# Performance work log

Hardware: AMD Instinct MI355X
Metric: run time of the kernel (lower is better)

Reference implementation:

```python
import jax, jax.numpy as jnp
import numpy as np

B, WIN, NN, NF, NH, NOUT = 4, 10, 10000, 8, 64, 1
N = B * WIN * NN          # stacked graph nodes
E = 3200000               # edges
EPS = 1e-5                # BatchNorm eps


def _gcn(x, edge_index, ew, W, b):
    # PyG GCNConv: linear first, then sym-normalized aggregation with self loops.
    xl = x @ W  # [N, H]
    loop = jnp.arange(N)
    row = jnp.concatenate([edge_index[0], loop])
    col = jnp.concatenate([edge_index[1], loop])
    w = jnp.concatenate([ew, jnp.ones((N,), ew.dtype)])
    deg = jax.ops.segment_sum(w, col, num_segments=N)
    dinv = jnp.where(deg > 0, jax.lax.rsqrt(deg), 0.0)
    norm = dinv[row] * w * dinv[col]
    out = jax.ops.segment_sum(norm[:, None] * xl[row], col, num_segments=N)
    return out + b


def _bn(x, g, bta):
    # training-mode BatchNorm1d (batch statistics, biased variance)
    m = x.mean(0)
    v = x.var(0)
    return (x - m) * jax.lax.rsqrt(v + EPS) * g + bta


def _lstm(xs, wih, whh, bih, bhh):
    # xs: [T, Bn, D]; PyTorch gate order i, f, g, o
    H = whh.shape[1]
    Bn = xs.shape[1]
    h0 = jnp.zeros((Bn, H), xs.dtype)
    c0 = jnp.zeros((Bn, H), xs.dtype)
    def step(carry, xt):
        h, c = carry
        gates = xt @ wih.T + bih + h @ whh.T + bhh
        i, f, g, o = jnp.split(gates, 4, axis=-1)
        c = jax.nn.sigmoid(f) * c + jax.nn.sigmoid(i) * jnp.tanh(g)
        h = jax.nn.sigmoid(o) * jnp.tanh(c)
        return (h, c), h
    (hn, cn), ys = jax.lax.scan(step, (h0, c0), xs)
    return ys, hn


def setup_inputs() -> dict:
    key = jax.random.key(0)
    ks = jax.random.split(key, 16)
    def rn(k, shape, s=0.05):
        return jax.random.normal(k, shape, jnp.float32) * s
    return {
        "x": jax.random.normal(ks[0], (N, NF), jnp.float32),
        "edge_index": jax.random.randint(ks[1], (2, E), 0, N),
        "edge_weight": jax.random.uniform(ks[2], (E,), jnp.float32),
        "c1_w": rn(ks[3], (NF, NH)), "c1_b": jnp.zeros((NH,), jnp.float32),
        "c2_w": rn(ks[4], (NH, NH)), "c2_b": jnp.zeros((NH,), jnp.float32),
        "bn1_g": jnp.ones((NH,), jnp.float32), "bn1_b": jnp.zeros((NH,), jnp.float32),
        "bn2_g": jnp.ones((NH,), jnp.float32), "bn2_b": jnp.zeros((NH,), jnp.float32),
        "l1_wih": rn(ks[5], (4 * NH, 2 * NH)), "l1_whh": rn(ks[6], (4 * NH, NH)),
        "l1_bih": jnp.zeros((4 * NH,), jnp.float32), "l1_bhh": jnp.zeros((4 * NH,), jnp.float32),
        "l2_wih": rn(ks[7], (4 * NH, NH)), "l2_whh": rn(ks[8], (4 * NH, NH)),
        "l2_bih": jnp.zeros((4 * NH,), jnp.float32), "l2_bhh": jnp.zeros((4 * NH,), jnp.float32),
        "fc1_w": rn(ks[9], (NH, 2 * NH + WIN * NF)), "fc1_b": jnp.zeros((NH,), jnp.float32),
        "fc2_w": rn(ks[10], (NOUT, NH)), "fc2_b": jnp.zeros((NOUT,), jnp.float32),
    }


def reference(x, edge_index, edge_weight, c1_w, c1_b, c2_w, c2_b,
              bn1_g, bn1_b, bn2_g, bn2_b,
              l1_wih, l1_whh, l1_bih, l1_bhh,
              l2_wih, l2_whh, l2_bih, l2_bhh,
              fc1_w, fc1_b, fc2_w, fc2_b):
    # skip connection: raw features per (batch,node) over the window
    skip = x.reshape(B, WIN, NN, NF).transpose(0, 2, 1, 3).reshape(B * NN, WIN * NF)
    # two GCN layers (dropout is identity in deterministic/eval reference)
    h1 = _bn(jax.nn.relu(_gcn(x, edge_index, edge_weight, c1_w, c1_b)), bn1_g, bn1_b)
    h2 = _bn(jax.nn.relu(_gcn(h1, edge_index, edge_weight, c2_w, c2_b)), bn2_g, bn2_b)
    xc = jnp.concatenate([h1, h2], axis=1)  # [N, 2H]
    xr = xc.reshape(B, WIN, NN, 2 * NH).transpose(1, 0, 2, 3).reshape(WIN, B * NN, 2 * NH)
    ys1, hn1 = _lstm(xr, l1_wih, l1_whh, l1_bih, l1_bhh)
    ys2, hn2 = _lstm(ys1, l2_wih, l2_whh, l2_bih, l2_bhh)
    z = jnp.concatenate([hn1, hn2, skip], axis=1)
    z = jax.nn.relu(z @ fc1_w.T + fc1_b)
    z = jax.nn.relu(z @ fc2_w.T + fc2_b)
    return z.reshape(-1)
```

## Files before the change

### kernel.cpp

```cpp
#include <hip/hip_runtime.h>
#include <math.h>

constexpr int BB     = 4;
constexpr int WINN   = 10;
constexpr int NNODES = 10000;
constexpr int NFEAT  = 8;
constexpr int NHID   = 64;
constexpr int NTOT   = BB * WINN * NNODES;
constexpr int NEDGE  = 3200000;
constexpr int NBN    = BB * NNODES;
constexpr float EPSBN = 1e-5f;

#define DEVFN static __device__ __forceinline__

typedef float f4 __attribute__((ext_vector_type(4)));
typedef short s8v __attribute__((ext_vector_type(8)));
typedef unsigned short ushort_t;
typedef unsigned int uint_t;

DEVFN float sigmoidf_(float x) { return 1.0f / (1.0f + __expf(-x)); }
DEVFN float tanhf_(float x) { return 2.0f / (1.0f + __expf(-2.0f * x)) - 1.0f; }
DEVFN ushort_t f2bf(float f) {
    uint_t x = __float_as_uint(f);
    return (ushort_t)((x + 0x7FFFu + ((x >> 16) & 1u)) >> 16);
}
DEVFN float bf2f(ushort_t u) { return __uint_as_float(((uint_t)u) << 16); }

__global__ void k_diag(float* out, float wsz, int n) {
    int i = blockIdx.x * 256 + threadIdx.x;
    if (i < n) out[i] = wsz;
}

__global__ void k_init(float* deg, int* cnt, float* sums) {
    int i = blockIdx.x * 256 + threadIdx.x;
    if (i < NTOT) { deg[i] = 1.0f; cnt[i] = 0; }
    if (i < 2048) sums[i] = 0.f;
}

__global__ void k_deg(const int* __restrict__ ei, const float* __restrict__ ew,
                      float* deg, int* cnt) {
    int e = blockIdx.x * 256 + threadIdx.x;
    if (e < NEDGE) {
        int c = ei[NEDGE + e];
        atomicAdd(&deg[c], ew[e]);
        atomicAdd(&cnt[c], 1);
    }
}

__global__ void k_dinv(float* deg) {
    int i = blockIdx.x * 256 + threadIdx.x;
    if (i < NTOT) { float d = deg[i]; deg[i] = (d > 0.f) ? rsqrtf(d) : 0.f; }
}

__global__ void k_scan1(const int* __restrict__ cnt, int* __restrict__ ptr, int* __restrict__ tmp) {
    __shared__ int sdat[256];
    int tid = threadIdx.x;
    int base = blockIdx.x * 1024 + tid * 4;
    int v0 = (base + 0 < NTOT) ? cnt[base + 0] : 0;
    int v1 = (base + 1 < NTOT) ? cnt[base + 1] : 0;
    int v2 = (base + 2 < NTOT) ? cnt[base + 2] : 0;
    int v3 = (base + 3 < NTOT) ? cnt[base + 3] : 0;
    int sum = v0 + v1 + v2 + v3;
    sdat[tid] = sum;
    __syncthreads();
    for (int ofs = 1; ofs < 256; ofs <<= 1) {
        int x = (tid >= ofs) ? sdat[tid - ofs] : 0;
        __syncthreads();
        sdat[tid] += x;
        __syncthreads();
    }
    int run = sdat[tid] - sum;
    if (base + 0 < NTOT) ptr[base + 0] = run; run += v0;
    if (base + 1 < NTOT) ptr[base + 1] = run; run += v1;
    if (base + 2 < NTOT) ptr[base + 2] = run; run += v2;
    if (base + 3 < NTOT) ptr[base + 3] = run;
    if (tid == 255) tmp[blockIdx.x] = sdat[255];
}

__global__ void k_scan2(int* tmp, int nb) {
    __shared__ int st[512];
    int tid = threadIdx.x;
    int v = (tid < nb) ? tmp[tid] : 0;
    st[tid] = v;
    __syncthreads();
    for (int ofs = 1; ofs < 512; ofs <<= 1) {
        int x = (tid >= ofs) ? st[tid - ofs] : 0;
        __syncthreads();
        st[tid] += x;
        __syncthreads();
    }
    if (tid < nb) tmp[tid] = st[tid] - v;
}

__global__ void k_scan3(int* __restrict__ ptr, int* __restrict__ cur, const int* __restrict__ tmp) {
    int i = blockIdx.x * 256 + threadIdx.x;
    if (i < NTOT) {
        int p = ptr[i] + tmp[i >> 10];
        ptr[i] = p;
        cur[i] = p;
    }
    if (i == 0) ptr[NTOT] = NEDGE;
}

__global__ void k_fill(const int* __restrict__ ei, const float* __restrict__ ew,
                       const float* __restrict__ dinv, int* __restrict__ cur,
                       int2* __restrict__ epack) {
    int e = blockIdx.x * 256 + threadIdx.x;
    if (e >= NEDGE) return;
    int row = ei[e], col = ei[NEDGE + e];
    float nv = dinv[row] * ew[e] * dinv[col];
    int pos = atomicAdd(&cur[col], 1);
    epack[pos] = make_int2(row, __float_as_int(nv));
}

__global__ void k_gather8(const int* __restrict__ ptr, const int2* __restrict__ epack,
                          const float* __restrict__ x, const float* __restrict__ dinv,
                          float* __restrict__ aggX) {
    int tid = threadIdx.x;
    int lane = tid & 63;
    int waveg = blockIdx.x * 4 + (tid >> 6);
    int g = lane >> 3, ch = lane & 7;
    int node = waveg * 8 + g;
    int beg = ptr[node], end = ptr[node + 1];
    float dv = dinv[node];
    float acc = dv * dv * x[node * 8 + ch];
    int e = beg;
    for (; e + 1 < end; e += 2) {
        int2 p0 = epack[e], p1 = epack[e + 1];
        acc = fmaf(__int_as_float(p0.y), x[p0.x * 8 + ch], acc);
        acc = fmaf(__int_as_float(p1.y), x[p1.x * 8 + ch], acc);
    }
    if (e < end) {
        int2 p = epack[e];
        acc = fmaf(__int_as_float(p.y), x[p.x * 8 + ch], acc);
    }
    aggX[node * 8 + ch] = acc;
}

__global__ void k_gather64(const int* __restrict__ ptr, const int2* __restrict__ epack,
                           const ushort_t* __restrict__ src, const float* __restrict__ dinv,
                           float* __restrict__ dst) {
    int lane = threadIdx.x & 63;
    int node = blockIdx.x * 4 + (threadIdx.x >> 6);
    int beg = ptr[node], end = ptr[node + 1];
    float dv = dinv[node];
    float acc = dv * dv * bf2f(src[(size_t)node * 64 + lane]);
    int e = beg;
    for (; e + 1 < end; e += 2) {
        int2 p0 = epack[e], p1 = epack[e + 1];
        acc = fmaf(__int_as_float(p0.y), bf2f(src[(size_t)p0.x * 64 + lane]), acc);
        acc = fmaf(__int_as_float(p1.y), bf2f(src[(size_t)p1.x * 64 + lane]), acc);
    }
    if (e < end) {
        int2 p = epack[e];
        acc = fmaf(__int_as_float(p.y), bf2f(src[(size_t)p.x * 64 + lane]), acc);
    }
    dst[(size_t)node * 64 + lane] = acc;
}

__global__ void k_lin1(const float* __restrict__ aggX, const float* __restrict__ W,
                       const float* __restrict__ bias, float* __restrict__ h1,
                       float* __restrict__ sums) {
    __shared__ float sW[NFEAT * NHID];
    int tid = threadIdx.x;
    sW[tid] = W[tid];
    sW[tid + 256] = W[tid + 256];
    __syncthreads();
    int c = tid & 63;
    float b = bias[c];
    float s = 0.f, sq = 0.f;
    int stride = gridDim.x * 256;
    for (int i = blockIdx.x * 256 + tid; i < NTOT * 64; i += stride) {
        int n = i >> 6;
        float acc = b;
#pragma unroll
        for (int f = 0; f < NFEAT; ++f) acc = fmaf(aggX[n * NFEAT + f], sW[f * NHID + c], acc);
        acc = acc > 0.f ? acc : 0.f;
        h1[i] = acc;
        s += acc;
        sq = fmaf(acc, acc, sq);
    }
    __shared__ float ls[4][64], lq[4][64];
    int w = tid >> 6;
    ls[w][c] = s; lq[w][c] = sq;
    __syncthreads();
    if (tid < 64) {
        atomicAdd(&sums[tid], ls[0][tid] + ls[1][tid] + ls[2][tid] + ls[3][tid]);
        atomicAdd(&sums[64 + tid], lq[0][tid] + lq[1][tid] + lq[2][tid] + lq[3][tid]);
    }
}

__global__ void k_bn_final(const float* __restrict__ sums, const float* __restrict__ g,
                           const float* __restrict__ b, float* __restrict__ ss) {
    int i = threadIdx.x;
    if (i >= 64) return;
    float mean = sums[i] * (1.0f / NTOT);
    float var = sums[64 + i] * (1.0f / NTOT) - mean * mean;
    float sc = g[i] * rsqrtf(var + EPSBN);
    ss[i] = sc;
    ss[64 + i] = b[i] - mean * sc;
}

__global__ void k_bn_final8(const float* __restrict__ sums8, const float* __restrict__ g,
                            const float* __restrict__ b, float* __restrict__ ss) {
    int i = threadIdx.x;
    if (i >= 64) return;
    float S = 0.f, Q = 0.f;
#pragma unroll
    for (int m = 0; m < 8; ++m) { S += sums8[m * 128 + i]; Q += sums8[m * 128 + 64 + i]; }
    float mean = S * (1.0f / NTOT);
    float var = Q * (1.0f / NTOT) - mean * mean;
    float sc = g[i] * rsqrtf(var + EPSBN);
    ss[i] = sc;
    ss[64 + i] = b[i] - mean * sc;
}

__global__ void k_bn1cast(const float* __restrict__ pre, const float* __restrict__ ss,
                          ushort_t* __restrict__ dst) {
    int c = threadIdx.x & 63;
    float sc = ss[c], sh = ss[64 + c];
    int stride = gridDim.x * 256;
    for (int i = blockIdx.x * 256 + threadIdx.x; i < NTOT * 64; i += stride)
        dst[i] = f2bf(fmaf(pre[i], sc, sh));
}

__global__ void k_lin2b(const float* __restrict__ io, const float* __restrict__ W2,
                        const float* __restrict__ bias, ushort_t* __restrict__ dst,
                        float* __restrict__ sums8) {
    __shared__ __align__(16) float srow[4][64];
    __shared__ float ls[4][64], lq[4][64];
    int lane = threadIdx.x & 63, wv = threadIdx.x >> 6;
    float wc[64];
#pragma unroll
    for (int h = 0; h < 64; ++h) wc[h] = W2[h * 64 + lane];
    float b = bias[lane];
    float s = 0.f, sq = 0.f;
    int wid = blockIdx.x * 4 + wv;
    int nw = gridDim.x * 4;
    for (int row = wid; row < NTOT; row += nw) {
        const float* hr = io + (size_t)row * 64;
        srow[wv][lane] = hr[lane];
        float acc = b;
#pragma unroll
        for (int h4 = 0; h4 < 16; ++h4) {
            float4 iv = *reinterpret_cast<const float4*>(&srow[wv][h4 * 4]);
            acc = fmaf(iv.x, wc[h4 * 4 + 0], acc);
            acc = fmaf(iv.y, wc[h4 * 4 + 1], acc);
            acc = fmaf(iv.z, wc[h4 * 4 + 2], acc);
            acc = fmaf(iv.w, wc[h4 * 4 + 3], acc);
        }
        acc = acc > 0.f ? acc : 0.f;
        dst[(size_t)row * 64 + lane] = f2bf(acc);
        s += acc;
        sq = fmaf(acc, acc, sq);
    }
    ls[wv][lane] = s; lq[wv][lane] = sq;
    __syncthreads();
    if (threadIdx.x < 64) {
        float S = ls[0][lane] + ls[1][lane] + ls[2][lane] + ls[3][lane];
        float Q = lq[0][lane] + lq[1][lane] + lq[2][lane] + lq[3][lane];
        float* d = sums8 + (blockIdx.x & 7) * 128;
        atomicAdd(&d[lane], S);
        atomicAdd(&d[64 + lane], Q);
    }
}

__global__ void k_prep(const float* __restrict__ wih1, const float* __restrict__ whh1,
                       const float* __restrict__ bih1, const float* __restrict__ bhh1,
                       const float* __restrict__ wih2, const float* __restrict__ whh2,
                       const float* __restrict__ bih2, const float* __restrict__ bhh2,
                       const float* __restrict__ fc1w,
                       float* wB1f, float* b1, ushort_t* wB2h, float* b2, float* fc1T) {
    int i = blockIdx.x * 256 + threadIdx.x;
    if (i < 256 * 192) {
        int n = i / 192, k = i - n * 192;
        wB1f[i] = (k < 128) ? wih1[n * 128 + k] : whh1[n * 64 + (k - 128)];
    }
    if (i < 256 * 128) {
        int n = i >> 7, k = i & 127;
        wB2h[i] = f2bf((k < 64) ? wih2[n * 64 + k] : whh2[n * 64 + (k - 64)]);
    }
    if (i < 208 * 64) {
        int k = i >> 6, o = i & 63;
        fc1T[i] = fc1w[o * 208 + k];
    }
    if (i < 256) { b1[i] = bih1[i] + bhh1[i]; b2[i] = bih2[i] + bhh2[i]; }
}

__global__ void k_fold2(float* __restrict__ wB1f, float* __restrict__ b1,
                        const float* __restrict__ ss2, ushort_t* __restrict__ wB1h) {
    int n = threadIdx.x;
    float acc = 0.f;
#pragma unroll
    for (int m = 0; m < 64; ++m) {
        float w = wB1f[n * 192 + 64 + m];
        acc = fmaf(w, ss2[64 + m], acc);
        wB1f[n * 192 + 64 + m] = w * ss2[m];
    }
    b1[n] += acc;
    __syncthreads();
    for (int j = n; j < 256 * 192; j += 256) wB1h[j] = f2bf(wB1f[j]);
}

__global__ __launch_bounds__(256, 2) void k_lstm_mfma4(
    const ushort_t* __restrict__ h1bf, const ushort_t* __restrict__ h2bf,
    const ushort_t* __restrict__ wB1, const ushort_t* __restrict__ wB2,
    const float* __restrict__ bs1, const float* __restrict__ bs2,
    float* __restrict__ hA, float* __restrict__ hB) {
    __shared__ ushort_t hx1[1024], hx2[1024];
    int tid = threadIdx.x;
    int lane = tid & 63, wv = tid >> 6;
    int c15 = lane & 15, g4 = lane >> 4;
    int g8 = g4 * 8;
    int bn0 = blockIdx.x * 16;
    int b = bn0 / NNODES, nn0 = bn0 - b * NNODES;

    for (int i = tid; i < 512; i += 256) { ((uint_t*)hx1)[i] = 0u; ((uint_t*)hx2)[i] = 0u; }

    s8v w1f[4][6], w2f[4][4];
#pragma unroll
    for (int j = 0; j < 4; ++j) {
        const ushort_t* base1 = wB1 + (size_t)((wv + 4 * j) * 16 + c15) * 192 + g8;
#pragma unroll
        for (int kk = 0; kk < 6; ++kk) w1f[j][kk] = *(const s8v*)(base1 + kk * 32);
        const ushort_t* base2 = wB2 + (size_t)((wv + 4 * j) * 16 + c15) * 128 + g8;
#pragma unroll
        for (int kk = 0; kk < 4; ++kk) w2f[j][kk] = *(const s8v*)(base2 + kk * 32);
    }
    float bi1[4], bi2[4];
#pragma unroll
    for (int j = 0; j < 4; ++j) {
        bi1[j] = bs1[(wv + 4 * j) * 16 + c15];
        bi2[j] = bs2[(wv + 4 * j) * 16 + c15];
    }
    float cA[4], cB[4];
#pragma unroll
    for (int q = 0; q < 4; ++q) { cA[q] = 0.f; cB[q] = 0.f; }

    int r7 = c15 & 7;
    int a_lo = c15 * 64 + ((g4 ^ r7) << 3);
    int a_hi = c15 * 64 + (((4 + g4) ^ r7) << 3);
    int u = wv * 16 + c15;
    int hxcol_hi = (u >> 3) << 3;
    int u7 = u & 7;

    __syncthreads();

    for (int t = 0; t < WINN; ++t) {
        size_t node = (size_t)((b * WINN + t) * NNODES + nn0 + c15) * 64 + g8;
        s8v a[6];
        a[0] = *(const s8v*)(h1bf + node);
        a[1] = *(const s8v*)(h1bf + node + 32);
        a[2] = *(const s8v*)(h2bf + node);
        a[3] = *(const s8v*)(h2bf + node + 32);
        a[4] = *(const s8v*)(&hx1[a_lo]);
        a[5] = *(const s8v*)(&hx1[a_hi]);

        f4 acc[4];
#pragma unroll
        for (int j = 0; j < 4; ++j) { f4 v = {bi1[j], bi1[j], bi1[j], bi1[j]}; acc[j] = v; }
#pragma unroll
        for (int j = 0; j < 4; ++j)
#pragma unroll
            for (int kk = 0; kk < 6; ++kk)
                acc[j] = __builtin_amdgcn_mfma_f32_16x16x32_bf16(a[kk], w1f[j][kk], acc[j], 0, 0, 0);
        __syncthreads();
#pragma unroll
        for (int q = 0; q < 4; ++q) {
            float ig = sigmoidf_(acc[0][q]);
            float fg = sigmoidf_(acc[1][q]);
            float gg = tanhf_(acc[2][q]);
            float og = sigmoidf_(acc[3][q]);
            float cv = fmaf(fg, cA[q], ig * gg);
            cA[q] = cv;
            float hv = og * tanhf_(cv);
            int rr = g4 * 4 + q;
            hx1[rr * 64 + (hxcol_hi ^ ((rr & 7) << 3)) + u7] = f2bf(hv);
        }
        __syncthreads();

        s8v r[4];
        r[0] = *(const s8v*)(&hx1[a_lo]);
        r[1] = *(const s8v*)(&hx1[a_hi]);
        r[2] = *(const s8v*)(&hx2[a_lo]);
        r[3] = *(const s8v*)(&hx2[a_hi]);
#pragma unroll
        for (int j = 0; j < 4; ++j) { f4 v = {bi2[j], bi2[j], bi2[j], bi2[j]}; acc[j] = v; }
#pragma unroll
        for (int j = 0; j < 4; ++j)
#pragma unroll
            for (int kk = 0; kk < 4; ++kk)
                acc[j] = __builtin_amdgcn_mfma_f32_16x16x32_bf16(r[kk], w2f[j][kk], acc[j], 0, 0, 0);
        __syncthreads();
#pragma unroll
        for (int q = 0; q < 4; ++q) {
            float ig = sigmoidf_(acc[0][q]);
            float fg = sigmoidf_(acc[1][q]);
            float gg = tanhf_(acc[2][q]);
            float og = sigmoidf_(acc[3][q]);
            float cv = fmaf(fg, cB[q], ig * gg);
            cB[q] = cv;
            float hv = og * tanhf_(cv);
            int rr = g4 * 4 + q;
            hx2[rr * 64 + (hxcol_hi ^ ((rr & 7) << 3)) + u7] = f2bf(hv);
        }
        __syncthreads();
    }
    for (int i = tid; i < 1024; i += 256) {
        int rr = i >> 6, uu = i & 63;
        int hw = rr * 64 + ((((uu >> 3) ^ (rr & 7)) << 3)) + (uu & 7);
        hA[(size_t)(bn0 + rr) * 64 + uu] = bf2f(hx1[hw]);
        hB[(size_t)(bn0 + rr) * 64 + uu] = bf2f(hx2[hw]);
    }
}

__global__ void k_head(const float* __restrict__ hA, const float* __restrict__ hB,
                       const float* __restrict__ x, const float* __restrict__ fc1T,
                       const float* __restrict__ fc1b, const float* __restrict__ fc2w,
                       const float* __restrict__ fc2b, float* __restrict__ out) {
    int lane = threadIdx.x & 63, wv = threadIdx.x >> 6;
    int bn = blockIdx.x * 4 + wv;
    __shared__ float sz[4][208];
    int b = bn / NNODES, nn = bn - b * NNODES;
    for (int k = lane; k < 208; k += 64) {
        float v;
        if (k < 64) v = hA[(size_t)bn * 64 + k];
        else if (k < 128) v = hB[(size_t)bn * 64 + (k - 64)];
        else {
            int kk = k - 128;
            int w = kk >> 3, f = kk & 7;
            v = x[(size_t)((b * WINN + w) * NNODES + nn) * NFEAT + f];
        }
        sz[wv][k] = v;
    }
    __syncthreads();
    float acc = fc1b[lane];
    for (int k = 0; k < 208; ++k) acc = fmaf(sz[wv][k], fc1T[k * 64 + lane], acc);
    acc = acc > 0.f ? acc : 0.f;
    float v = acc * fc2w[lane];
#pragma unroll
    for (int m = 32; m >= 1; m >>= 1) v += __shfl_xor(v, m, 64);
    if (lane == 0) {
        float z = v + fc2b[0];
        out[bn] = z > 0.f ? z : 0.f;
    }
}

extern "C" void kernel_launch(void* const* d_in, const int* in_sizes, int n_in,
                              void* d_out, int out_size, void* d_ws, size_t ws_size,
                              hipStream_t stream) {
    const float* x     = (const float*)d_in[0];
    const int*   ei    = (const int*)d_in[1];
    const float* ew    = (const float*)d_in[2];
    const float* c1w   = (const float*)d_in[3];
    const float* c1b   = (const float*)d_in[4];
    const float* c2w   = (const float*)d_in[5];
    const float* c2b   = (const float*)d_in[6];
    const float* bn1g  = (const float*)d_in[7];
    const float* bn1b  = (const float*)d_in[8];
    const float* bn2g  = (const float*)d_in[9];
    const float* bn2b  = (const float*)d_in[10];
    const float* wih1  = (const float*)d_in[11];
    const float* whh1  = (const float*)d_in[12];
    const float* bih1  = (const float*)d_in[13];
    const float* bhh1  = (const float*)d_in[14];
    const float* wih2  = (const float*)d_in[15];
    const float* whh2  = (const float*)d_in[16];
    const float* bih2  = (const float*)d_in[17];
    const float* bhh2  = (const float*)d_in[18];
    const float* fc1w  = (const float*)d_in[19];
    const float* fc1b  = (const float*)d_in[20];
    const float* fc2w  = (const float*)d_in[21];
    const float* fc2b  = (const float*)d_in[22];
    float* out = (float*)d_out;

    float* ws = (float*)d_ws;
    size_t off = 0;
    auto A = [&](size_t n) { float* p = ws + off; off += n; return p; };
    float* dinv   = A(NTOT);
    float* aggX   = A((size_t)NTOT * NFEAT);
    float* big    = A((size_t)NTOT * 64);
    ushort_t* h1bf = (ushort_t*)A((size_t)NTOT * 32);
    ushort_t* h2bf = (ushort_t*)A((size_t)NTOT * 32);

    size_t uoff = off;
    float* hA = A((size_t)NBN * 64);
    float* hB = A((size_t)NBN * 64);
    A(2 * (size_t)NEDGE + 2 * NTOT + 2 - 2 * (size_t)NBN * 64);
    int2* epack = (int2*)(ws + uoff);
    int*  ptr   = (int*)(epack + NEDGE);
    int*  cur   = ptr + NTOT + 1;

    float* wB1f = A(256 * 192);
    ushort_t* wB1h = (ushort_t*)A(256 * 96);
    ushort_t* wB2h = (ushort_t*)A(256 * 64);
    float* b1   = A(256);
    float* b2   = A(256);
    float* fc1T = A(208 * 64);
    float* sums = A(2048);
    float* ss1  = A(128);
    float* ss2  = A(128);
    float* scanTmpF = A(512);
    int* scanTmp = (int*)scanTmpF;

    if (ws_size < off * sizeof(float)) {
        k_diag<<<(out_size + 255) / 256, 256, 0, stream>>>(out, (float)ws_size, out_size);
        return;
    }

    constexpr int SCAN_NB = (NTOT + 1023) / 1024;

    k_init<<<(NTOT + 255) / 256, 256, 0, stream>>>(dinv, cur, sums);
    k_deg<<<NEDGE / 256, 256, 0, stream>>>(ei, ew, dinv, cur);
    k_dinv<<<(NTOT + 255) / 256, 256, 0, stream>>>(dinv);
    k_scan1<<<SCAN_NB, 256, 0, stream>>>(cur, ptr, scanTmp);
    k_scan2<<<1, 512, 0, stream>>>(scanTmp, SCAN_NB);
    k_scan3<<<(NTOT + 255) / 256, 256, 0, stream>>>(ptr, cur, scanTmp);
    k_fill<<<NEDGE / 256, 256, 0, stream>>>(ei, ew, dinv, cur, epack);
    k_prep<<<192, 256, 0, stream>>>(wih1, whh1, bih1, bhh1, wih2, whh2, bih2, bhh2,
                                    fc1w, wB1f, b1, wB2h, b2, fc1T);

    k_gather8<<<NTOT / 8 / 4, 256, 0, stream>>>(ptr, epack, x, dinv, aggX);
    k_lin1<<<512, 256, 0, stream>>>(aggX, c1w, c1b, big, sums);
    k_bn_final<<<1, 64, 0, stream>>>(sums, bn1g, bn1b, ss1);
    k_bn1cast<<<2048, 256, 0, stream>>>(big, ss1, h1bf);

    k_gather64<<<NTOT / 4, 256, 0, stream>>>(ptr, epack, h1bf, dinv, big);
    k_lin2b<<<2048, 256, 0, stream>>>(big, c2w, c2b, h2bf, sums + 128);
    k_bn_final8<<<1, 64, 0, stream>>>(sums + 128, bn2g, bn2b, ss2);
    k_fold2<<<1, 256, 0, stream>>>(wB1f, b1, ss2, wB1h);

    k_lstm_mfma4<<<NBN / 16, 256, 0, stream>>>(h1bf, h2bf, wB1h, wB2h, b1, b2, hA, hB);

    k_head<<<NBN / 4, 256, 0, stream>>>(hA, hB, x, fc1T, fc1b, fc2w, fc2b, out);
}
```

Before: 1.217 ms.

## Privatize CSR build counters into 8 partitions and compute degree from CSR

Replaces the float and int atomic degree and count pass with a single integer histogram split across 8 partitioned counter copies, chosen by block index, to spread atomic contention. Degree is then computed deterministically from the built CSR by a segmented reduction, and the per-edge normalization moves into the gather kernels, which now also load dinv[row] for every edge. This removes the float atomics and the dinv kernel. In exchange it adds 8x counter memory and initialization, an extra CSR pass, and an extra random dinv load per edge in both gathers.

```diff
diff --git a/kernel.cpp b/kernel.cpp
--- a/kernel.cpp
+++ b/kernel.cpp
@@ -31,36 +31,34 @@
     if (i < n) out[i] = wsz;
 }
 
-__global__ void k_init(float* deg, int* cnt, float* sums) {
+__global__ void k_init(int* cntP, float* sums) {
     int i = blockIdx.x * 256 + threadIdx.x;
-    if (i < NTOT) { deg[i] = 1.0f; cnt[i] = 0; }
+    if (i < 8 * NTOT) cntP[i] = 0;
     if (i < 2048) sums[i] = 0.f;
 }
 
-__global__ void k_deg(const int* __restrict__ ei, const float* __restrict__ ew,
-                      float* deg, int* cnt) {
+__global__ void k_hist(const int* __restrict__ ei, int* __restrict__ cntP) {
     int e = blockIdx.x * 256 + threadIdx.x;
-    if (e < NEDGE) {
-        int c = ei[NEDGE + e];
-        atomicAdd(&deg[c], ew[e]);
-        atomicAdd(&cnt[c], 1);
-    }
-}
-
-__global__ void k_dinv(float* deg) {
-    int i = blockIdx.x * 256 + threadIdx.x;
-    if (i < NTOT) { float d = deg[i]; deg[i] = (d > 0.f) ? rsqrtf(d) : 0.f; }
-}
-
-__global__ void k_scan1(const int* __restrict__ cnt, int* __restrict__ ptr, int* __restrict__ tmp) {
+    int p = blockIdx.x & 7;
+    if (e < NEDGE) atomicAdd(&cntP[p * NTOT + ei[NEDGE + e]], 1);
+}
+
+__global__ void k_scan1(const int* __restrict__ cntP, int* __restrict__ ptr, int* __restrict__ tmp) {
     __shared__ int sdat[256];
     int tid = threadIdx.x;
     int base = blockIdx.x * 1024 + tid * 4;
-    int v0 = (base + 0 < NTOT) ? cnt[base + 0] : 0;
-    int v1 = (base + 1 < NTOT) ? cnt[base + 1] : 0;
-    int v2 = (base + 2 < NTOT) ? cnt[base + 2] : 0;
-    int v3 = (base + 3 < NTOT) ? cnt[base + 3] : 0;
-    int sum = v0 + v1 + v2 + v3;
+    int v[4];
+#pragma unroll
+    for (int j = 0; j < 4; ++j) {
+        int idx = base + j;
+        int s = 0;
+        if (idx < NTOT) {
+#pragma unroll
+            for (int p = 0; p < 8; ++p) s += cntP[p * NTOT + idx];
+        }
+        v[j] = s;
+    }
+    int sum = v[0] + v[1] + v[2] + v[3];
     sdat[tid] = sum;
     __syncthreads();
     for (int ofs = 1; ofs < 256; ofs <<= 1) {
@@ -70,9 +68,9 @@
         __syncthreads();
     }
     int run = sdat[tid] - sum;
-    if (base + 0 < NTOT) ptr[base + 0] = run; run += v0;
-    if (base + 1 < NTOT) ptr[base + 1] = run; run += v1;
-    if (base + 2 < NTOT) ptr[base + 2] = run; run += v2;
+    if (base + 0 < NTOT) ptr[base + 0] = run; run += v[0];
+    if (base + 1 < NTOT) ptr[base + 1] = run; run += v[1];
+    if (base + 2 < NTOT) ptr[base + 2] = run; run += v[2];
     if (base + 3 < NTOT) ptr[base + 3] = run;
     if (tid == 255) tmp[blockIdx.x] = sdat[255];
 }
@@ -92,25 +90,46 @@
     if (tid < nb) tmp[tid] = st[tid] - v;
 }
 
-__global__ void k_scan3(int* __restrict__ ptr, int* __restrict__ cur, const int* __restrict__ tmp) {
+__global__ void k_scan3(int* __restrict__ ptr, int* __restrict__ cntP, const int* __restrict__ tmp) {
     int i = blockIdx.x * 256 + threadIdx.x;
     if (i < NTOT) {
-        int p = ptr[i] + tmp[i >> 10];
-        ptr[i] = p;
-        cur[i] = p;
+        int p0 = ptr[i] + tmp[i >> 10];
+        ptr[i] = p0;
+        int run = p0;
+#pragma unroll
+        for (int p = 0; p < 8; ++p) {
+            int c = cntP[p * NTOT + i];
+            cntP[p * NTOT + i] = run;
+            run += c;
+        }
     }
     if (i == 0) ptr[NTOT] = NEDGE;
 }
 
 __global__ void k_fill(const int* __restrict__ ei, const float* __restrict__ ew,
-                       const float* __restrict__ dinv, int* __restrict__ cur,
-                       int2* __restrict__ epack) {
+                       int* __restrict__ cur8, int2* __restrict__ epack) {
     int e = blockIdx.x * 256 + threadIdx.x;
     if (e >= NEDGE) return;
+    int p = blockIdx.x & 7;
     int row = ei[e], col = ei[NEDGE + e];
-    float nv = dinv[row] * ew[e] * dinv[col];
-    int pos = atomicAdd(&cur[col], 1);
-    epack[pos] = make_int2(row, __float_as_int(nv));
+    int pos = atomicAdd(&cur8[p * NTOT + col], 1);
+    epack[pos] = make_int2(row, __float_as_int(ew[e]));
+}
+
+__global__ void k_degcsr(const int* __restrict__ ptr, const int2* __restrict__ epack,
+                         float* __restrict__ dinv) {
+    int tid = threadIdx.x;
+    int lane = tid & 63;
+    int waveg = blockIdx.x * 4 + (tid >> 6);
+    int g = lane >> 3, sub = lane & 7;
+    int node = waveg * 8 + g;
+    int beg = ptr[node], end = ptr[node + 1];
+    float s = 0.f;
+    for (int e = beg + sub; e < end; e += 8) s += __int_as_float(epack[e].y);
+    s += __shfl_xor(s, 1, 64);
+    s += __shfl_xor(s, 2, 64);
+    s += __shfl_xor(s, 4, 64);
+    if (sub == 0) dinv[node] = rsqrtf(1.0f + s);
 }
 
 __global__ void k_gather8(const int* __restrict__ ptr, const int2* __restrict__ epack,
@@ -123,18 +142,18 @@
     int node = waveg * 8 + g;
     int beg = ptr[node], end = ptr[node + 1];
     float dv = dinv[node];
-    float acc = dv * dv * x[node * 8 + ch];
+    float accE = 0.f;
     int e = beg;
     for (; e + 1 < end; e += 2) {
         int2 p0 = epack[e], p1 = epack[e + 1];
-        acc = fmaf(__int_as_float(p0.y), x[p0.x * 8 + ch], acc);
-        acc = fmaf(__int_as_float(p1.y), x[p1.x * 8 + ch], acc);
+        accE = fmaf(dinv[p0.x] * __int_as_float(p0.y), x[p0.x * 8 + ch], accE);
+        accE = fmaf(dinv[p1.x] * __int_as_float(p1.y), x[p1.x * 8 + ch], accE);
     }
     if (e < end) {
         int2 p = epack[e];
-        acc = fmaf(__int_as_float(p.y), x[p.x * 8 + ch], acc);
-    }
-    aggX[node * 8 + ch] = acc;
+        accE = fmaf(dinv[p.x] * __int_as_float(p.y), x[p.x * 8 + ch], accE);
+    }
+    aggX[node * 8 + ch] = dv * fmaf(dv, x[node * 8 + ch], accE);
 }
 
 __global__ void k_gather64(const int* __restrict__ ptr, const int2* __restrict__ epack,
@@ -144,18 +163,18 @@
     int node = blockIdx.x * 4 + (threadIdx.x >> 6);
     int beg = ptr[node], end = ptr[node + 1];
     float dv = dinv[node];
-    float acc = dv * dv * bf2f(src[(size_t)node * 64 + lane]);
+    float accE = 0.f;
     int e = beg;
     for (; e + 1 < end; e += 2) {
         int2 p0 = epack[e], p1 = epack[e + 1];
-        acc = fmaf(__int_as_float(p0.y), bf2f(src[(size_t)p0.x * 64 + lane]), acc);
-        acc = fmaf(__int_as_float(p1.y), bf2f(src[(size_t)p1.x * 64 + lane]), acc);
+        accE = fmaf(dinv[p0.x] * __int_as_float(p0.y), bf2f(src[(size_t)p0.x * 64 + lane]), accE);
+        accE = fmaf(dinv[p1.x] * __int_as_float(p1.y), bf2f(src[(size_t)p1.x * 64 + lane]), accE);
     }
     if (e < end) {
         int2 p = epack[e];
-        acc = fmaf(__int_as_float(p.y), bf2f(src[(size_t)p.x * 64 + lane]), acc);
-    }
-    dst[(size_t)node * 64 + lane] = acc;
+        accE = fmaf(dinv[p.x] * __int_as_float(p.y), bf2f(src[(size_t)p.x * 64 + lane]), accE);
+    }
+    dst[(size_t)node * 64 + lane] = dv * fmaf(dv, bf2f(src[(size_t)node * 64 + lane]), accE);
 }
 
 __global__ void k_lin1(const float* __restrict__ aggX, const float* __restrict__ W,
@@ -486,10 +505,10 @@
     size_t uoff = off;
     float* hA = A((size_t)NBN * 64);
     float* hB = A((size_t)NBN * 64);
-    A(2 * (size_t)NEDGE + 2 * NTOT + 2 - 2 * (size_t)NBN * 64);
+    A(2 * (size_t)NEDGE + (NTOT + 1) + 8 * (size_t)NTOT - 2 * (size_t)NBN * 64);
     int2* epack = (int2*)(ws + uoff);
     int*  ptr   = (int*)(epack + NEDGE);
-    int*  cur   = ptr + NTOT + 1;
+    int*  cntP  = ptr + NTOT + 1;
 
     float* wB1f = A(256 * 192);
     ushort_t* wB1h = (ushort_t*)A(256 * 96);
@@ -510,13 +529,13 @@
 
     constexpr int SCAN_NB = (NTOT + 1023) / 1024;
 
-    k_init<<<(NTOT + 255) / 256, 256, 0, stream>>>(dinv, cur, sums);
-    k_deg<<<NEDGE / 256, 256, 0, stream>>>(ei, ew, dinv, cur);
-    k_dinv<<<(NTOT + 255) / 256, 256, 0, stream>>>(dinv);
-    k_scan1<<<SCAN_NB, 256, 0, stream>>>(cur, ptr, scanTmp);
+    k_init<<<8 * NTOT / 256, 256, 0, stream>>>(cntP, sums);
+    k_hist<<<NEDGE / 256, 256, 0, stream>>>(ei, cntP);
+    k_scan1<<<SCAN_NB, 256, 0, stream>>>(cntP, ptr, scanTmp);
     k_scan2<<<1, 512, 0, stream>>>(scanTmp, SCAN_NB);
-    k_scan3<<<(NTOT + 255) / 256, 256, 0, stream>>>(ptr, cur, scanTmp);
-    k_fill<<<NEDGE / 256, 256, 0, stream>>>(ei, ew, dinv, cur, epack);
+    k_scan3<<<(NTOT + 255) / 256, 256, 0, stream>>>(ptr, cntP, scanTmp);
+    k_fill<<<NEDGE / 256, 256, 0, stream>>>(ei, ew, cntP, epack);
+    k_degcsr<<<NTOT / 8 / 4, 256, 0, stream>>>(ptr, epack, dinv);
     k_prep<<<192, 256, 0, stream>>>(wih1, whh1, bih1, bhh1, wih2, whh2, bih2, bhh2,
                                     fc1w, wB1f, b1, wB2h, b2, fc1T);
 
```

Result: faster. 1.160 ms (-4.6%).
